# Optimization experiments

Measured on AMD Instinct MI355X. Metric: run time of the kernel, lower is better.

Reference implementation:

```python
import jax, jax.numpy as jnp
import numpy as np

# MORR all-pass ring parameters (MORRConfig_20um defaults: attenuation / self-coupling)
A_MORR = 0.8578
R_MORR = 0.8578
KS = 3       # kernel_size
MB = 8       # miniblock (circulant block size)
BN_EPS = 1e-5


def mrr_roundtrip_phase_to_tr(phi):
    # through-port transmission of an all-pass microring vs roundtrip phase
    c = jnp.cos(phi)
    num = A_MORR * A_MORR - 2.0 * A_MORR * R_MORR * c + R_MORR * R_MORR
    den = 1.0 - 2.0 * A_MORR * R_MORR * c + (A_MORR * R_MORR) ** 2
    return num / den


def setup_inputs() -> dict:
    key = jax.random.key(0)
    k1, k2 = jax.random.split(key, 2)
    B, C, H, W = 64, 64, 32, 32
    outC = 64
    q = (C * KS * KS + MB - 1) // MB   # grid_dim_x = 72
    p = (outC + MB - 1) // MB          # grid_dim_y = 8
    x = jax.random.normal(k1, (B, C, H, W), jnp.float32)
    weight = jax.random.normal(k2, (p, q, MB), jnp.float32) * 0.05  # circulant eigen-vectors per block
    gamma = jnp.ones((outC,), jnp.float32)   # BatchNorm2d weight
    beta = jnp.zeros((outC,), jnp.float32)   # BatchNorm2d bias
    return {"x": x, "weight": weight, "gamma": gamma, "beta": beta}


def reference(x, weight, gamma, beta):
    B, C, H, W = x.shape
    p, q, mb = weight.shape
    outC = gamma.shape[0]
    Ho, Wo = H, W  # stride=1, padding=1, ks=3
    L = Ho * Wo
    # im2col (torch F.unfold ordering: C major, then kh, kw)
    xp = jnp.pad(x, ((0, 0), (0, 0), (1, 1), (1, 1)))
    cols = jnp.stack([xp[:, :, i:i + Ho, j:j + Wo]
                      for i in range(KS) for j in range(KS)], axis=2)  # [B,C,9,Ho,Wo]
    cols = cols.reshape(B, C * KS * KS, L).transpose(0, 2, 1)          # [B,L,C*k*k]
    assert C * KS * KS == q * mb, "patch dim must pad to q*mb"
    s = cols.reshape(B, L, q, mb)
    s = s * s  # optical intensity (power) fed into the MORR
    # block-circulant weight: Wc[p,q,i,j] = weight[p,q,(i-j) mod mb]
    i_idx = jnp.arange(mb)
    idx = (i_idx[:, None] - i_idx[None, :]) % mb
    Wc = weight[:, :, idx]                                             # [p,q,mb,mb]
    # accumulated roundtrip phase per output node
    phase = jnp.einsum('blqj,pqij->blpi', s, Wc)                       # [B,L,p,mb]
    tr = mrr_roundtrip_phase_to_tr(phase)
    out = tr.reshape(B, L, p * mb)[:, :, :outC]                        # truncate to out_channel
    out = out.transpose(0, 2, 1).reshape(B, outC, Ho, Wo)
    # BatchNorm2d (training mode: batch statistics) + Hardtanh(-1, 1)
    mean = out.mean(axis=(0, 2, 3), keepdims=True)
    var = out.var(axis=(0, 2, 3), keepdims=True)
    y = (out - mean) * jax.lax.rsqrt(var + BN_EPS)
    y = y * gamma[None, :, None, None] + beta[None, :, None, None]
    return jnp.clip(y, -1.0, 1.0)
```

## Files before the change

### kernel.cpp

```cpp
#include <hip/hip_runtime.h>


#define A_MORR 0.8578f
#define R_MORR 0.8578f
#define TR_C1 (A_MORR * A_MORR + R_MORR * R_MORR)
#define TR_C2 (-2.0f * A_MORR * R_MORR)
#define TR_C3 (1.0f + (A_MORR * R_MORR) * (A_MORR * R_MORR))
#define BN_EPS 1e-5f

#define NPIX 65536
#define X2_LO 26112
#define SMEM_BYTES 52224

typedef __attribute__((ext_vector_type(8))) short bf16x8;
typedef __attribute__((ext_vector_type(16))) float f32x16;

__device__ __forceinline__ void bf16split(float s, unsigned short& h, unsigned short& l) {
    union { float f; unsigned u; } cv; cv.f = s;
    unsigned r = (cv.u + 0x7fffu + ((cv.u >> 16) & 1u)) & 0xffff0000u;
    h = (unsigned short)(r >> 16);
    union { unsigned u; float f; } hv; hv.u = r;
    float lo = s - hv.f;
    cv.f = lo;
    unsigned r2 = cv.u + 0x7fffu + ((cv.u >> 16) & 1u);
    l = (unsigned short)(r2 >> 16);
}

__global__ __launch_bounds__(256) void prep_kernel(const float* __restrict__ w,
                                                   char* __restrict__ wfrag,
                                                   float* __restrict__ stats) {
    int gtid = blockIdx.x * 256 + threadIdx.x;
    if (gtid < 128) stats[gtid] = 0.0f;
    if (gtid < 36864) {
        int j    = gtid & 7;
        int lane = (gtid >> 3) & 63;
        int okm  = gtid >> 9;
        int mt   = okm & 1;
        int ks   = (okm >> 1) & 3;
        int off  = okm >> 3;
        int oc   = mt * 32 + (lane & 31);
        int c    = ks * 16 + (lane >> 5) * 8 + j;
        int kg   = c * 9 + off;
        float val = w[(oc >> 3) * 576 + (kg >> 3) * 8 + ((oc - kg) & 7)];
        unsigned short h, l;
        bf16split(val, h, l);
        ((unsigned short*)(wfrag + okm * 2048))[lane * 8 + j] = h;
        ((unsigned short*)(wfrag + okm * 2048 + 1024))[lane * 8 + j] = l;
    }
}

__global__ __launch_bounds__(256, 2) void conv_kernel(const float* __restrict__ x,
                                                      const char* __restrict__ wfrag,
                                                      float* __restrict__ out,
                                                      float* __restrict__ stats) {
    const int rt  = blockIdx.x;
    const int b   = blockIdx.y;
    const int tid = threadIdx.x;

    __shared__ __align__(16) char smem[SMEM_BYTES];

    if (tid < 192) {
        int prec = tid & 1;
        int g    = (tid >> 1) & 7;
        int rc   = tid >> 4;
        int r    = rc >> 1;
        int c    = (rc & 1) ? 33 : 0;
        *(uint4*)(smem + prec * X2_LO + ((r * 34 + c) << 7) + (g << 4)) = uint4{0, 0, 0, 0};
    }

    {
        const int co  = tid & 7;
        const int chp = tid >> 3;
        const float* xb = x + (size_t)(b * 64 + 2 * chp) * 1024;
#pragma unroll
        for (int rr = 0; rr < 6; ++rr) {
            int gr = rt * 4 - 1 + rr;
            float4 a0 = {0.f, 0.f, 0.f, 0.f}, a1 = {0.f, 0.f, 0.f, 0.f};
            if (gr >= 0 && gr < 32) {
                const float* rp = xb + gr * 32 + co * 4;
                a0 = *(const float4*)rp;
                a1 = *(const float4*)(rp + 1024);
            }
            float s0[4] = {a0.x * a0.x, a0.y * a0.y, a0.z * a0.z, a0.w * a0.w};
            float s1[4] = {a1.x * a1.x, a1.y * a1.y, a1.z * a1.z, a1.w * a1.w};
#pragma unroll
            for (int i = 0; i < 4; ++i) {
                unsigned short h0, l0, h1, l1;
                bf16split(s0[i], h0, l0);
                bf16split(s1[i], h1, l1);
                int c    = 1 + co * 4 + i;
                int base = ((rr * 34 + c) << 7) + ((((2 * chp) >> 3) ^ (c & 7)) << 4)
                         + ((chp & 3) << 2);
                *(unsigned*)(smem + base)         = (unsigned)h0 | ((unsigned)h1 << 16);
                *(unsigned*)(smem + X2_LO + base) = (unsigned)l0 | ((unsigned)l1 << 16);
            }
        }
    }
    __syncthreads();

    const int lane = tid & 63;
    const int wv   = tid >> 6;
    const int wmt  = wv & 1;
    const int py   = wv >> 1;
    const int col  = lane & 31;
    const int hs   = lane >> 5;

    f32x16 acc0, acc1;
#pragma unroll
    for (int i = 0; i < 16; ++i) { acc0[i] = 0.f; acc1[i] = 0.f; }

#pragma unroll
    for (int di = 0; di < 3; ++di) {
#pragma unroll
        for (int dj = 0; dj < 3; ++dj) {
            const int off = di * 3 + dj;
            const int c   = col + dj;
            const int c7  = c & 7;
            const int rc0 = (((py * 2 + di) * 34 + c) << 7);
            const int rc1 = rc0 + (34 << 7);
#pragma unroll
            for (int ks = 0; ks < 4; ++ks) {
                const int gsw = ((ks * 2 + hs) ^ c7) << 4;
                bf16x8 bh0 = *(const bf16x8*)(smem + rc0 + gsw);
                bf16x8 bl0 = *(const bf16x8*)(smem + X2_LO + rc0 + gsw);
                bf16x8 bh1 = *(const bf16x8*)(smem + rc1 + gsw);
                bf16x8 bl1 = *(const bf16x8*)(smem + X2_LO + rc1 + gsw);
                const char* wp = wfrag + ((off * 4 + ks) * 2 + wmt) * 2048 + lane * 16;
                bf16x8 ah = *(const bf16x8*)wp;
                bf16x8 al = *(const bf16x8*)(wp + 1024);
                acc0 = __builtin_amdgcn_mfma_f32_32x32x16_bf16(ah, bh0, acc0, 0, 0, 0);
                acc1 = __builtin_amdgcn_mfma_f32_32x32x16_bf16(ah, bh1, acc1, 0, 0, 0);
                acc0 = __builtin_amdgcn_mfma_f32_32x32x16_bf16(ah, bl0, acc0, 0, 0, 0);
                acc1 = __builtin_amdgcn_mfma_f32_32x32x16_bf16(ah, bl1, acc1, 0, 0, 0);
                acc0 = __builtin_amdgcn_mfma_f32_32x32x16_bf16(al, bh0, acc0, 0, 0, 0);
                acc1 = __builtin_amdgcn_mfma_f32_32x32x16_bf16(al, bh1, acc1, 0, 0, 0);
            }
        }
    }

    float* red1 = (float*)smem;
    float* red2 = red1 + 64 * 66;
    float ps1 = 0.f, ps2 = 0.f;
    const int ocr = tid & 63, q = tid >> 6;
    const size_t outbase = ((size_t)b * 64 + wmt * 32) * 1024 + rt * 128;

#pragma unroll
    for (int nt = 0; nt < 2; ++nt) {
        __syncthreads();
        const int pxr = (py * 2 + nt) * 32 + col;
#pragma unroll
        for (int r = 0; r < 16; ++r) {
            int ocl   = (r & 3) + 8 * (r >> 2) + 4 * hs;
            float phi = nt ? acc1[r] : acc0[r];
            float cph = __cosf(phi);
            float t   = fmaf(TR_C2, cph, TR_C1) / fmaf(TR_C2, cph, TR_C3);
            out[outbase + (size_t)ocl * 1024 + pxr] = t;
            int ri = (wmt * 32 + ocl) * 66 + py * 32 + col;
            red1[ri] = t;
            red2[ri] = t * t;
        }
        __syncthreads();
        float s1 = 0.f, s2 = 0.f;
#pragma unroll
        for (int i = 0; i < 16; ++i) {
            s1 += red1[ocr * 66 + q * 16 + i];
            s2 += red2[ocr * 66 + q * 16 + i];
        }
        ps1 += s1; ps2 += s2;
    }
    __syncthreads();
    red1[tid] = ps1;
    red2[tid] = ps2;
    __syncthreads();
    if (tid < 64) {
        float s1 = red1[tid] + red1[tid + 64] + red1[tid + 128] + red1[tid + 192];
        float s2 = red2[tid] + red2[tid + 64] + red2[tid + 128] + red2[tid + 192];
        atomicAdd(&stats[tid], s1);
        atomicAdd(&stats[64 + tid], s2);
    }
}

__global__ __launch_bounds__(64) void stats_kernel(const float* __restrict__ stats,
                                                   const float* __restrict__ gamma,
                                                   const float* __restrict__ beta,
                                                   float* __restrict__ ss) {
    int oc = threadIdx.x;
    if (oc >= 64) return;
    const float invN = 1.0f / (float)NPIX;
    float mean = stats[oc] * invN;
    float var  = stats[64 + oc] * invN - mean * mean;
    float sc   = gamma[oc] * rsqrtf(var + BN_EPS);
    ss[oc]      = sc;
    ss[64 + oc] = beta[oc] - mean * sc;
}

__global__ __launch_bounds__(256) void norm_kernel(float* __restrict__ out,
                                                   const float* __restrict__ ss) {
    int i = blockIdx.x * 256 + threadIdx.x;
    float4 v = ((float4*)out)[i];
    int oc = (i >> 8) & 63;
    float sc = ss[oc];
    float sh = ss[64 + oc];
    v.x = fminf(1.0f, fmaxf(-1.0f, fmaf(v.x, sc, sh)));
    v.y = fminf(1.0f, fmaxf(-1.0f, fmaf(v.y, sc, sh)));
    v.z = fminf(1.0f, fmaxf(-1.0f, fmaf(v.z, sc, sh)));
    v.w = fminf(1.0f, fmaxf(-1.0f, fmaf(v.w, sc, sh)));
    ((float4*)out)[i] = v;
}

extern "C" void kernel_launch(void* const* d_in, const int* in_sizes, int n_in,
                              void* d_out, int out_size, void* d_ws, size_t ws_size,
                              hipStream_t stream) {
    const float* x     = (const float*)d_in[0];
    const float* w     = (const float*)d_in[1];
    const float* gamma = (const float*)d_in[2];
    const float* beta  = (const float*)d_in[3];
    float* out = (float*)d_out;

    char*  wfrag = (char*)d_ws;
    float* stats = (float*)((char*)d_ws + 147456);
    float* ss    = stats + 128;

    hipLaunchKernelGGL(prep_kernel, dim3(144), dim3(256), 0, stream, w, wfrag, stats);
    hipLaunchKernelGGL(conv_kernel, dim3(8, 64), dim3(256), 0, stream, x, wfrag, out, stats);
    hipLaunchKernelGGL(stats_kernel, dim3(1), dim3(64), 0, stream, stats, gamma, beta, ss);
    hipLaunchKernelGGL(norm_kernel, dim3(4096), dim3(256), 0, stream, out, ss);
}
```

Baseline: 49.88 us.

## Fuse BatchNorm stats and normalize into conv via cooperative grid sync

Merges the stats and normalization kernels into the conv kernel. Activations stay in registers, and a cooperative-launch grid barrier waits for the global statistics before normalized, clipped outputs are written once. This removes the extra read and write of the full output tensor and two kernel launches. It requires all 512 blocks to be co-resident (2 per CU), adds grid-sync cost, and also stops unrolling the di/dj conv loops, which may cost some instruction scheduling.

New measurement: 79.20 us. 1.59x slower.

```diff
diff --git a/kernel.cpp b/kernel.cpp
--- a/kernel.cpp
+++ b/kernel.cpp
@@ -1,4 +1,7 @@
 #include <hip/hip_runtime.h>
+#include <hip/hip_cooperative_groups.h>
+
+namespace cg = cooperative_groups;
 
 
 #define A_MORR 0.8578f
@@ -52,7 +55,9 @@
 __global__ __launch_bounds__(256, 2) void conv_kernel(const float* __restrict__ x,
                                                       const char* __restrict__ wfrag,
                                                       float* __restrict__ out,
-                                                      float* __restrict__ stats) {
+                                                      float* __restrict__ stats,
+                                                      const float* __restrict__ gamma,
+                                                      const float* __restrict__ beta) {
     const int rt  = blockIdx.x;
     const int b   = blockIdx.y;
     const int tid = threadIdx.x;
@@ -109,25 +114,26 @@
 #pragma unroll
     for (int i = 0; i < 16; ++i) { acc0[i] = 0.f; acc1[i] = 0.f; }
 
-#pragma unroll
+    const char* wbase = wfrag + wmt * 2048 + (size_t)lane * 16;
+
+#pragma unroll 1
     for (int di = 0; di < 3; ++di) {
-#pragma unroll
+#pragma unroll 1
         for (int dj = 0; dj < 3; ++dj) {
             const int off = di * 3 + dj;
             const int c   = col + dj;
             const int c7  = c & 7;
-            const int rc0 = (((py * 2 + di) * 34 + c) << 7);
-            const int rc1 = rc0 + (34 << 7);
+            const char* sb0 = smem + (((py * 2 + di) * 34 + c) << 7);
+            const char* wp  = wbase + off * 16384;
 #pragma unroll
             for (int ks = 0; ks < 4; ++ks) {
-                const int gsw = ((ks * 2 + hs) ^ c7) << 4;
-                bf16x8 bh0 = *(const bf16x8*)(smem + rc0 + gsw);
-                bf16x8 bl0 = *(const bf16x8*)(smem + X2_LO + rc0 + gsw);
-                bf16x8 bh1 = *(const bf16x8*)(smem + rc1 + gsw);
-                bf16x8 bl1 = *(const bf16x8*)(smem + X2_LO + rc1 + gsw);
-                const char* wp = wfrag + ((off * 4 + ks) * 2 + wmt) * 2048 + lane * 16;
-                bf16x8 ah = *(const bf16x8*)wp;
-                bf16x8 al = *(const bf16x8*)(wp + 1024);
+                const int g = ((ks * 2 + hs) ^ c7) << 4;
+                bf16x8 bh0 = *(const bf16x8*)(sb0 + g);
+                bf16x8 bl0 = *(const bf16x8*)(sb0 + X2_LO + g);
+                bf16x8 bh1 = *(const bf16x8*)(sb0 + (34 << 7) + g);
+                bf16x8 bl1 = *(const bf16x8*)(sb0 + X2_LO + (34 << 7) + g);
+                bf16x8 ah  = *(const bf16x8*)(wp + ks * 4096);
+                bf16x8 al  = *(const bf16x8*)(wp + ks * 4096 + 1024);
                 acc0 = __builtin_amdgcn_mfma_f32_32x32x16_bf16(ah, bh0, acc0, 0, 0, 0);
                 acc1 = __builtin_amdgcn_mfma_f32_32x32x16_bf16(ah, bh1, acc1, 0, 0, 0);
                 acc0 = __builtin_amdgcn_mfma_f32_32x32x16_bf16(ah, bl0, acc0, 0, 0, 0);
@@ -138,74 +144,75 @@
         }
     }
 
+#pragma unroll
+    for (int r = 0; r < 16; ++r) {
+        float c0 = __cosf(acc0[r]);
+        float c1 = __cosf(acc1[r]);
+        acc0[r] = fmaf(TR_C2, c0, TR_C1) / fmaf(TR_C2, c0, TR_C3);
+        acc1[r] = fmaf(TR_C2, c1, TR_C1) / fmaf(TR_C2, c1, TR_C3);
+    }
+
     float* red1 = (float*)smem;
     float* red2 = red1 + 64 * 66;
-    float ps1 = 0.f, ps2 = 0.f;
-    const int ocr = tid & 63, q = tid >> 6;
-    const size_t outbase = ((size_t)b * 64 + wmt * 32) * 1024 + rt * 128;
-
-#pragma unroll
-    for (int nt = 0; nt < 2; ++nt) {
-        __syncthreads();
-        const int pxr = (py * 2 + nt) * 32 + col;
-#pragma unroll
-        for (int r = 0; r < 16; ++r) {
-            int ocl   = (r & 3) + 8 * (r >> 2) + 4 * hs;
-            float phi = nt ? acc1[r] : acc0[r];
-            float cph = __cosf(phi);
-            float t   = fmaf(TR_C2, cph, TR_C1) / fmaf(TR_C2, cph, TR_C3);
-            out[outbase + (size_t)ocl * 1024 + pxr] = t;
-            int ri = (wmt * 32 + ocl) * 66 + py * 32 + col;
-            red1[ri] = t;
-            red2[ri] = t * t;
-        }
-        __syncthreads();
+    float* ssc  = red2 + 64 * 66;
+    float* ssh  = ssc + 64;
+
+    __syncthreads();
+#pragma unroll
+    for (int r = 0; r < 16; ++r) {
+        int ocl  = (r & 3) + 8 * (r >> 2) + 4 * hs;
+        float t0 = acc0[r], t1 = acc1[r];
+        int ri = (wmt * 32 + ocl) * 66 + py * 32 + col;
+        red1[ri] = t0 + t1;
+        red2[ri] = t0 * t0 + t1 * t1;
+    }
+    __syncthreads();
+    {
+        const int ocr = tid & 63, q = tid >> 6;
         float s1 = 0.f, s2 = 0.f;
 #pragma unroll
         for (int i = 0; i < 16; ++i) {
             s1 += red1[ocr * 66 + q * 16 + i];
             s2 += red2[ocr * 66 + q * 16 + i];
         }
-        ps1 += s1; ps2 += s2;
-    }
-    __syncthreads();
-    red1[tid] = ps1;
-    red2[tid] = ps2;
-    __syncthreads();
+        __syncthreads();
+        red1[tid] = s1;
+        red2[tid] = s2;
+        __syncthreads();
+        if (tid < 64) {
+            float a1 = red1[tid] + red1[tid + 64] + red1[tid + 128] + red1[tid + 192];
+            float a2 = red2[tid] + red2[tid + 64] + red2[tid + 128] + red2[tid + 192];
+            atomicAdd(&stats[tid], a1);
+            atomicAdd(&stats[64 + tid], a2);
+        }
+    }
+
+    cg::this_grid().sync();
+
     if (tid < 64) {
-        float s1 = red1[tid] + red1[tid + 64] + red1[tid + 128] + red1[tid + 192];
-        float s2 = red2[tid] + red2[tid + 64] + red2[tid + 128] + red2[tid + 192];
-        atomicAdd(&stats[tid], s1);
-        atomicAdd(&stats[64 + tid], s2);
-    }
-}
-
-__global__ __launch_bounds__(64) void stats_kernel(const float* __restrict__ stats,
-                                                   const float* __restrict__ gamma,
-                                                   const float* __restrict__ beta,
-                                                   float* __restrict__ ss) {
-    int oc = threadIdx.x;
-    if (oc >= 64) return;
-    const float invN = 1.0f / (float)NPIX;
-    float mean = stats[oc] * invN;
-    float var  = stats[64 + oc] * invN - mean * mean;
-    float sc   = gamma[oc] * rsqrtf(var + BN_EPS);
-    ss[oc]      = sc;
-    ss[64 + oc] = beta[oc] - mean * sc;
-}
-
-__global__ __launch_bounds__(256) void norm_kernel(float* __restrict__ out,
-                                                   const float* __restrict__ ss) {
-    int i = blockIdx.x * 256 + threadIdx.x;
-    float4 v = ((float4*)out)[i];
-    int oc = (i >> 8) & 63;
-    float sc = ss[oc];
-    float sh = ss[64 + oc];
-    v.x = fminf(1.0f, fmaxf(-1.0f, fmaf(v.x, sc, sh)));
-    v.y = fminf(1.0f, fmaxf(-1.0f, fmaf(v.y, sc, sh)));
-    v.z = fminf(1.0f, fmaxf(-1.0f, fmaf(v.z, sc, sh)));
-    v.w = fminf(1.0f, fmaxf(-1.0f, fmaf(v.w, sc, sh)));
-    ((float4*)out)[i] = v;
+        float s1 = __hip_atomic_load(&stats[tid], __ATOMIC_RELAXED, __HIP_MEMORY_SCOPE_AGENT);
+        float s2 = __hip_atomic_load(&stats[64 + tid], __ATOMIC_RELAXED, __HIP_MEMORY_SCOPE_AGENT);
+        const float invN = 1.0f / (float)NPIX;
+        float mean = s1 * invN;
+        float var  = s2 * invN - mean * mean;
+        float sc   = gamma[tid] * rsqrtf(var + BN_EPS);
+        ssc[tid] = sc;
+        ssh[tid] = beta[tid] - mean * sc;
+    }
+    __syncthreads();
+
+    const size_t outbase = ((size_t)b * 64 + wmt * 32) * 1024 + rt * 128;
+#pragma unroll
+    for (int r = 0; r < 16; ++r) {
+        int ocl  = (r & 3) + 8 * (r >> 2) + 4 * hs;
+        float sc = ssc[wmt * 32 + ocl];
+        float sh = ssh[wmt * 32 + ocl];
+        float y0 = fminf(1.0f, fmaxf(-1.0f, fmaf(acc0[r], sc, sh)));
+        float y1 = fminf(1.0f, fmaxf(-1.0f, fmaf(acc1[r], sc, sh)));
+        size_t o = outbase + (size_t)ocl * 1024 + py * 64 + col;
+        out[o]      = y0;
+        out[o + 32] = y1;
+    }
 }
 
 extern "C" void kernel_launch(void* const* d_in, const int* in_sizes, int n_in,
@@ -219,10 +226,11 @@
 
     char*  wfrag = (char*)d_ws;
     float* stats = (float*)((char*)d_ws + 147456);
-    float* ss    = stats + 128;
 
     hipLaunchKernelGGL(prep_kernel, dim3(144), dim3(256), 0, stream, w, wfrag, stats);
-    hipLaunchKernelGGL(conv_kernel, dim3(8, 64), dim3(256), 0, stream, x, wfrag, out, stats);
-    hipLaunchKernelGGL(stats_kernel, dim3(1), dim3(64), 0, stream, stats, gamma, beta, ss);
-    hipLaunchKernelGGL(norm_kernel, dim3(4096), dim3(256), 0, stream, out, ss);
-}
+
+    void* cargs[] = { (void*)&x, (void*)&wfrag, (void*)&out,
+                      (void*)&stats, (void*)&gamma, (void*)&beta };
+    hipLaunchCooperativeKernel((const void*)conv_kernel, dim3(8, 64), dim3(256),
+                               cargs, 0, stream);
+}
```
